# Performance work log

Measured on AMD Instinct MI355X. Metric: run time of the kernel, lower is better.

## Reference

```python
import jax, jax.numpy as jnp
import numpy as np

N = 50000      # nodes
E = 800000     # edges (avg degree 16)
D = 256        # d_model
H = 8          # heads
C = D // H     # per-head channels = 32
DE = 64        # edge feature dim
NEG_SLOPE = 0.2
EPS = 1e-5


def setup_inputs() -> dict:
    key = jax.random.key(0)
    ks = jax.random.split(key, 12)
    s = 0.05
    return {
        "x": jax.random.normal(ks[0], (N, D), jnp.float32),
        "edge_attr": jax.random.normal(ks[1], (E, DE), jnp.float32),
        "edge_index": jax.random.randint(ks[2], (2, E), 0, N, dtype=jnp.int32),
        # GATv2Conv params (torch Linear layout: [out, in])
        "W_l": jax.random.normal(ks[3], (H * C, D), jnp.float32) * s,   # lin_l (source)
        "b_l": jnp.zeros((H * C,), jnp.float32),
        "W_r": jax.random.normal(ks[4], (H * C, D), jnp.float32) * s,   # lin_r (target)
        "b_r": jnp.zeros((H * C,), jnp.float32),
        "W_e": jax.random.normal(ks[5], (H * C, DE), jnp.float32) * s,  # lin_edge (no bias)
        "att": jax.random.normal(ks[6], (H, C), jnp.float32) * s,       # attention vector a
        "W_res": jax.random.normal(ks[7], (H * C, D), jnp.float32) * s, # residual Linear (no bias)
        "bias": jnp.zeros((H * C,), jnp.float32),                        # conv output bias
        "gamma": jnp.ones((D,), jnp.float32),                            # LayerNorm weight
        "beta": jnp.zeros((D,), jnp.float32),                            # LayerNorm bias
    }


def reference(x, edge_attr, W_l, b_l, W_r, b_r, W_e, att, W_res, bias, gamma, beta, edge_index):
    src = edge_index[0]  # j (messages flow source -> target)
    dst = edge_index[1]  # i

    xl = (x @ W_l.T + b_l).reshape(N, H, C)   # source transform
    xr = (x @ W_r.T + b_r).reshape(N, H, C)   # target transform
    ee = (edge_attr @ W_e.T).reshape(E, H, C)  # edge embedding

    # GATv2 attention logits per edge/head
    g = jax.nn.leaky_relu(xl[src] + xr[dst] + ee, NEG_SLOPE)  # [E, H, C]
    alpha = jnp.einsum("ehc,hc->eh", g, att)                   # [E, H]

    # segment softmax over incoming edges of each target node
    amax = jax.ops.segment_max(alpha, dst, num_segments=N)     # [N, H] (-inf for empty)
    ealpha = jnp.exp(alpha - amax[dst])
    denom = jax.ops.segment_sum(ealpha, dst, num_segments=N)   # [N, H]
    alpha = ealpha / jnp.where(denom > 0, denom, 1.0)[dst]

    # weighted message aggregation (scatter-add)
    msg = xl[src] * alpha[:, :, None]                          # [E, H, C]
    out = jax.ops.segment_sum(msg, dst, num_segments=N)        # [N, H, C]

    out = out.reshape(N, H * C) + x @ W_res.T + bias           # concat heads + residual + bias

    # LayerNorm over last dim
    mu = out.mean(-1, keepdims=True)
    var = ((out - mu) ** 2).mean(-1, keepdims=True)
    return (out - mu) * jax.lax.rsqrt(var + EPS) * gamma + beta
```

## Files before the change

kernel.cpp:

```cpp
#include <hip/hip_runtime.h>

#define N_NODES 50000
#define N_EDGES 800000
#define D_MODEL 256
#define H_HEADS 8
#define C_CH 32
#define DE_DIM 64
#define NEG_SLOPE 0.2f
#define LN_EPS 1e-5f
#define TILES (N_EDGES / 64)
#define AGG_K 32

typedef float  f32x4  __attribute__((ext_vector_type(4)));
typedef short  bf16x8 __attribute__((ext_vector_type(8)));

static __device__ __forceinline__ unsigned short f2bf(float f) {
    unsigned int u = __float_as_uint(f);
    u += 0x7fffu + ((u >> 16) & 1u);
    return (unsigned short)(u >> 16);
}
static __device__ __forceinline__ float bf2f(unsigned short s) {
    return __uint_as_float(((unsigned int)s) << 16);
}
static __device__ __forceinline__ bf16x8 load_cvt8(const float* __restrict__ p) {
    float4 a = *(const float4*)p;
    float4 b = *(const float4*)(p + 4);
    bf16x8 r;
    r[0] = (short)f2bf(a.x); r[1] = (short)f2bf(a.y);
    r[2] = (short)f2bf(a.z); r[3] = (short)f2bf(a.w);
    r[4] = (short)f2bf(b.x); r[5] = (short)f2bf(b.y);
    r[6] = (short)f2bf(b.z); r[7] = (short)f2bf(b.w);
    return r;
}

__global__ __launch_bounds__(256) void cvt_bf16_kernel(const float* __restrict__ in,
                                                       unsigned short* __restrict__ out,
                                                       int n8) {
    int g = blockIdx.x * 256 + threadIdx.x;
    if (g < n8) {
        bf16x8 v = load_cvt8(in + (size_t)g * 8);
        *(bf16x8*)(out + (size_t)g * 8) = v;
    }
}

__global__ __launch_bounds__(256) void node_gemm(const unsigned short* __restrict__ xbf,
                                                 const unsigned short* __restrict__ Wbf,
                                                 const float* __restrict__ bl,
                                                 const float* __restrict__ br,
                                                 unsigned short* __restrict__ xl,
                                                 unsigned short* __restrict__ xr,
                                                 float* __restrict__ res) {
    int tid = threadIdx.x;
    int lane = tid & 63, wv = tid >> 6;
    int quad = lane >> 4, l15 = lane & 15;
    int rowTile = blockIdx.x * 64;
    int which = blockIdx.y;
    const unsigned short* W = Wbf + (size_t)which * 65536;
    int colBase = wv * 64;

    f32x4 acc[4][4];
#pragma unroll
    for (int r = 0; r < 4; r++)
#pragma unroll
        for (int c = 0; c < 4; c++) acc[r][c] = (f32x4){0.f, 0.f, 0.f, 0.f};

#pragma unroll 1
    for (int k8 = 0; k8 < 8; ++k8) {
        int kb = k8 * 32 + quad * 8;
        bf16x8 af[4], bfr[4];
#pragma unroll
        for (int r = 0; r < 4; r++) {
            int row = rowTile + r * 16 + l15;
            if (row > N_NODES - 1) row = N_NODES - 1;
            af[r] = *(const bf16x8*)(xbf + (size_t)row * D_MODEL + kb);
        }
#pragma unroll
        for (int c = 0; c < 4; c++) {
            int col = colBase + c * 16 + l15;
            bfr[c] = *(const bf16x8*)(W + (size_t)col * D_MODEL + kb);
        }
#pragma unroll
        for (int r = 0; r < 4; r++)
#pragma unroll
            for (int c = 0; c < 4; c++)
                acc[r][c] = __builtin_amdgcn_mfma_f32_16x16x32_bf16(af[r], bfr[c], acc[r][c], 0, 0, 0);
    }

    float bv[4];
#pragma unroll
    for (int c = 0; c < 4; c++) {
        int col = colBase + c * 16 + l15;
        bv[c] = (which == 0) ? bl[col] : (which == 1 ? br[col] : 0.f);
    }
#pragma unroll
    for (int r = 0; r < 4; r++) {
#pragma unroll
        for (int g = 0; g < 4; g++) {
            int row = rowTile + r * 16 + quad * 4 + g;
            if (row < N_NODES) {
#pragma unroll
                for (int c = 0; c < 4; c++) {
                    int col = colBase + c * 16 + l15;
                    float v = acc[r][c][g] + bv[c];
                    size_t idx = (size_t)row * D_MODEL + col;
                    if (which == 0)      xl[idx] = f2bf(v);
                    else if (which == 1) xr[idx] = f2bf(v);
                    else                 res[idx] = v;
                }
            }
        }
    }
}

__global__ __launch_bounds__(256) void edge_logits(const float* __restrict__ edge_attr,
                                                   const float* __restrict__ We,
                                                   const float* __restrict__ att,
                                                   const int* __restrict__ srcIdx,
                                                   const int* __restrict__ dstIdx,
                                                   const int* __restrict__ posOf,
                                                   const unsigned short* __restrict__ xl,
                                                   const unsigned short* __restrict__ xr,
                                                   float* __restrict__ alphaP) {
    __shared__ short weS[2048 * 8];
    __shared__ float attS[256];
    __shared__ short aS[4][128 * 8];

    int tid = threadIdx.x;
    int lane = tid & 63, wv = tid >> 6;
    int quad = lane >> 4, l15 = lane & 15;

    for (int g = tid; g < 2048; g += 256) {
        int c = g >> 7, kq = (g >> 6) & 1, ln = g & 63;
        int o = c * 16 + (ln & 15);
        int k = kq * 32 + (ln >> 4) * 8;
        bf16x8 v = load_cvt8(We + o * DE_DIM + k);
        *(bf16x8*)&weS[g * 8] = v;
    }
    if (tid < 256) attS[tid] = att[tid];
    __syncthreads();

    for (int tile = blockIdx.x; tile < TILES; tile += gridDim.x) {
        int e0 = tile * 64 + wv * 16;
#pragma unroll
        for (int kq = 0; kq < 2; ++kq) {
            int e = e0 + l15;
            int k = kq * 32 + quad * 8;
            bf16x8 v = load_cvt8(edge_attr + (size_t)e * DE_DIM + k);
            *(bf16x8*)&aS[wv][(kq * 64 + lane) * 8] = v;
        }
        int srcv[4], dstv[4], posv[4];
#pragma unroll
        for (int r = 0; r < 4; r++) {
            int e = e0 + quad * 4 + r;
            srcv[r] = srcIdx[e];
            dstv[r] = dstIdx[e];
            posv[r] = posOf[e];
        }
        __syncthreads();

        bf16x8 a0 = *(bf16x8*)&aS[wv][(0 * 64 + lane) * 8];
        bf16x8 a1 = *(bf16x8*)&aS[wv][(1 * 64 + lane) * 8];

        float pa[4][8];
#pragma unroll
        for (int r = 0; r < 4; r++)
#pragma unroll
            for (int h = 0; h < 8; h++) pa[r][h] = 0.f;

#pragma unroll
        for (int c = 0; c < 16; c++) {
            bf16x8 b0 = *(bf16x8*)&weS[((c * 2 + 0) * 64 + lane) * 8];
            bf16x8 b1 = *(bf16x8*)&weS[((c * 2 + 1) * 64 + lane) * 8];
            f32x4 ee = (f32x4){0.f, 0.f, 0.f, 0.f};
            ee = __builtin_amdgcn_mfma_f32_16x16x32_bf16(a0, b0, ee, 0, 0, 0);
            ee = __builtin_amdgcn_mfma_f32_16x16x32_bf16(a1, b1, ee, 0, 0, 0);
            int col = c * 16 + l15;
            float attv = attS[col];
#pragma unroll
            for (int r = 0; r < 4; r++) {
                float xlv = bf2f(xl[(size_t)srcv[r] * D_MODEL + col]);
                float xrv = bf2f(xr[(size_t)dstv[r] * D_MODEL + col]);
                float t = ee[r] + xlv + xrv;
                t = (t > 0.f) ? t : NEG_SLOPE * t;
                pa[r][c >> 1] += t * attv;
            }
        }
#pragma unroll
        for (int r = 0; r < 4; r++)
#pragma unroll
            for (int h = 0; h < 8; h++) {
                float v = pa[r][h];
                v += __shfl_xor(v, 1);
                v += __shfl_xor(v, 2);
                v += __shfl_xor(v, 4);
                v += __shfl_xor(v, 8);
                pa[r][h] = v;
            }
        if (l15 == 0) {
#pragma unroll
            for (int r = 0; r < 4; r++) {
#pragma unroll
                for (int h = 0; h < 8; h++)
                    alphaP[(size_t)posv[r] * 8 + h] = pa[r][h];
            }
        }
        __syncthreads();
    }
}

__global__ __launch_bounds__(256) void hist_kernel(const int* __restrict__ dstIdx,
                                                   int* __restrict__ cnt) {
    int e = blockIdx.x * 256 + threadIdx.x;
    if (e < N_EDGES) atomicAdd(&cnt[dstIdx[e]], 1);
}

__global__ __launch_bounds__(1024) void scan_kernel(const int* __restrict__ cnt,
                                                    int* __restrict__ off,
                                                    int* __restrict__ woff) {
    const int CHUNK = 49;
    int tid = threadIdx.x;
    int base = tid * CHUNK;
    int local[CHUNK];
    int sum = 0;
#pragma unroll
    for (int j = 0; j < CHUNK; ++j) {
        int idx = base + j;
        int v = (idx < N_NODES) ? cnt[idx] : 0;
        local[j] = sum;
        sum += v;
    }
    int lane = tid & 63, wv = tid >> 6;
    int s = sum;
#pragma unroll
    for (int ofs = 1; ofs < 64; ofs <<= 1) {
        int t2 = __shfl_up(s, ofs);
        if (lane >= ofs) s += t2;
    }
    __shared__ int wsum[16];
    __shared__ int woffS[16];
    if (lane == 63) wsum[wv] = s;
    __syncthreads();
    if (tid == 0) {
        int a = 0;
#pragma unroll
        for (int i = 0; i < 16; ++i) { woffS[i] = a; a += wsum[i]; }
    }
    __syncthreads();
    int excl = woffS[wv] + (s - sum);
#pragma unroll
    for (int j = 0; j < CHUNK; ++j) {
        int idx = base + j;
        if (idx < N_NODES) {
            int v = excl + local[j];
            off[idx] = v;
            woff[idx] = v;
        }
    }
    if (tid == 0) off[N_NODES] = N_EDGES;
}

__global__ __launch_bounds__(256) void scatter_kernel(const int* __restrict__ srcIdx,
                                                      const int* __restrict__ dstIdx,
                                                      int* __restrict__ woff,
                                                      int* __restrict__ posOf,
                                                      int* __restrict__ srcP) {
    int e = blockIdx.x * 256 + threadIdx.x;
    if (e < N_EDGES) {
        int pos = atomicAdd(&woff[dstIdx[e]], 1);
        posOf[e] = pos;
        srcP[pos] = srcIdx[e];
    }
}

__global__ __launch_bounds__(256) void aggregate_ln(const int* __restrict__ off,
                                                    const int* __restrict__ srcP,
                                                    const float* __restrict__ alphaP,
                                                    const unsigned short* __restrict__ xl,
                                                    const float* __restrict__ res,
                                                    const float* __restrict__ biasc,
                                                    const float* __restrict__ gamma,
                                                    const float* __restrict__ beta,
                                                    float* __restrict__ out) {
    int i = blockIdx.x;
    int t = threadIdx.x;
    int h = t >> 5;
    int beg = off[i], end = off[i + 1];

    __shared__ float wS[AGG_K * 8];
    __shared__ int srcS[AGG_K];

    float s = 0.f, acc = 0.f;
    for (int ch = beg; ch < end; ch += AGG_K) {
        int n = min(AGG_K, end - ch);
        __syncthreads();
        if (t < n * 8) wS[t] = __expf(alphaP[(size_t)ch * 8 + t]);
        if (t < n)     srcS[t] = srcP[ch + t];
        __syncthreads();
#pragma unroll 4
        for (int p = 0; p < n; ++p) {
            float w = wS[p * 8 + h];
            s += w;
            acc += w * bf2f(xl[(size_t)srcS[p] * D_MODEL + t]);
        }
    }
    float v = (end > beg) ? (acc / s) : 0.f;
    v += res[(size_t)i * D_MODEL + t] + biasc[t];

    __shared__ float rs[4], rq[4];
    float sum = v, sq = v * v;
#pragma unroll
    for (int msk = 32; msk >= 1; msk >>= 1) {
        sum += __shfl_xor(sum, msk);
        sq  += __shfl_xor(sq, msk);
    }
    int lane = t & 63, wv = t >> 6;
    __syncthreads();
    if (lane == 0) { rs[wv] = sum; rq[wv] = sq; }
    __syncthreads();
    float tot  = rs[0] + rs[1] + rs[2] + rs[3];
    float totq = rq[0] + rq[1] + rq[2] + rq[3];
    float mu  = tot * (1.f / 256.f);
    float var = totq * (1.f / 256.f) - mu * mu;
    var = fmaxf(var, 0.f);
    float inv = rsqrtf(var + LN_EPS);
    out[(size_t)i * D_MODEL + t] = (v - mu) * inv * gamma[t] + beta[t];
}

extern "C" void kernel_launch(void* const* d_in, const int* in_sizes, int n_in,
                              void* d_out, int out_size, void* d_ws, size_t ws_size,
                              hipStream_t stream) {
    const float* x         = (const float*)d_in[0];
    const float* edge_attr = (const float*)d_in[1];
    const int*   edge_index= (const int*)d_in[2];
    const float* Wl        = (const float*)d_in[3];
    const float* bl        = (const float*)d_in[4];
    const float* Wr        = (const float*)d_in[5];
    const float* br        = (const float*)d_in[6];
    const float* We        = (const float*)d_in[7];
    const float* att       = (const float*)d_in[8];
    const float* Wres      = (const float*)d_in[9];
    const float* biasc     = (const float*)d_in[10];
    const float* gamma     = (const float*)d_in[11];
    const float* beta      = (const float*)d_in[12];
    const int* srcIdx = edge_index;
    const int* dstIdx = edge_index + N_EDGES;
    float* out = (float*)d_out;

    char* ws = (char*)d_ws;
    unsigned short* xl  = (unsigned short*)ws;
    unsigned short* xr  = xl + (size_t)N_NODES * D_MODEL;
    unsigned short* xbf = xr + (size_t)N_NODES * D_MODEL;
    unsigned short* Wbf = xbf + (size_t)N_NODES * D_MODEL;
    float* res    = (float*)(Wbf + 3 * 65536);
    float* alphaP = res + (size_t)N_NODES * D_MODEL;
    int* cnt   = (int*)(alphaP + (size_t)N_EDGES * 8);
    int* off   = cnt + N_NODES;
    int* woff  = off + (N_NODES + 1);
    int* posOf = woff + N_NODES;
    int* srcP  = posOf + N_EDGES;
    (void)ws_size; (void)n_in; (void)in_sizes; (void)out_size;

    hipMemsetAsync(cnt, 0, N_NODES * sizeof(int), stream);

    cvt_bf16_kernel<<<(N_NODES * D_MODEL / 8 + 255) / 256, 256, 0, stream>>>(x, xbf, N_NODES * D_MODEL / 8);
    cvt_bf16_kernel<<<32, 256, 0, stream>>>(Wl,   Wbf,             65536 / 8);
    cvt_bf16_kernel<<<32, 256, 0, stream>>>(Wr,   Wbf + 65536,     65536 / 8);
    cvt_bf16_kernel<<<32, 256, 0, stream>>>(Wres, Wbf + 2 * 65536, 65536 / 8);

    dim3 g1((N_NODES + 63) / 64, 3);
    node_gemm<<<g1, 256, 0, stream>>>(xbf, Wbf, bl, br, xl, xr, res);

    hist_kernel<<<(N_EDGES + 255) / 256, 256, 0, stream>>>(dstIdx, cnt);
    scan_kernel<<<1, 1024, 0, stream>>>(cnt, off, woff);
    scatter_kernel<<<(N_EDGES + 255) / 256, 256, 0, stream>>>(srcIdx, dstIdx, woff, posOf, srcP);

    edge_logits<<<1280, 256, 0, stream>>>(edge_attr, We, att, srcIdx, dstIdx, posOf, xl, xr, alphaP);

    aggregate_ln<<<N_NODES, 256, 0, stream>>>(off, srcP, alphaP, xl, res,
                                              biasc, gamma, beta, out);
}
```

Baseline: 887.4 us.

## Swap MFMA operands in edge_logits to drop LDS staging and syncs

```diff
diff --git a/kernel.cpp b/kernel.cpp
--- a/kernel.cpp
+++ b/kernel.cpp
@@ -123,7 +123,6 @@
                                                    float* __restrict__ alphaP) {
     __shared__ short weS[2048 * 8];
     __shared__ float attS[256];
-    __shared__ short aS[4][128 * 8];
 
     int tid = threadIdx.x;
     int lane = tid & 63, wv = tid >> 6;
@@ -141,70 +140,49 @@
 
     for (int tile = blockIdx.x; tile < TILES; tile += gridDim.x) {
         int e0 = tile * 64 + wv * 16;
-#pragma unroll
-        for (int kq = 0; kq < 2; ++kq) {
-            int e = e0 + l15;
-            int k = kq * 32 + quad * 8;
-            bf16x8 v = load_cvt8(edge_attr + (size_t)e * DE_DIM + k);
-            *(bf16x8*)&aS[wv][(kq * 64 + lane) * 8] = v;
-        }
-        int srcv[4], dstv[4], posv[4];
-#pragma unroll
-        for (int r = 0; r < 4; r++) {
-            int e = e0 + quad * 4 + r;
-            srcv[r] = srcIdx[e];
-            dstv[r] = dstIdx[e];
-            posv[r] = posOf[e];
-        }
-        __syncthreads();
-
-        bf16x8 a0 = *(bf16x8*)&aS[wv][(0 * 64 + lane) * 8];
-        bf16x8 a1 = *(bf16x8*)&aS[wv][(1 * 64 + lane) * 8];
-
-        float pa[4][8];
-#pragma unroll
-        for (int r = 0; r < 4; r++)
-#pragma unroll
-            for (int h = 0; h < 8; h++) pa[r][h] = 0.f;
+        int e = e0 + l15;
+        bf16x8 a0 = load_cvt8(edge_attr + (size_t)e * DE_DIM + quad * 8);
+        bf16x8 a1 = load_cvt8(edge_attr + (size_t)e * DE_DIM + 32 + quad * 8);
+        int se = srcIdx[e];
+        int de = dstIdx[e];
+        int pos = posOf[e];
+        const unsigned short* xlr = xl + (size_t)se * D_MODEL;
+        const unsigned short* xrr = xr + (size_t)de * D_MODEL;
+
+        float pa[8];
+#pragma unroll
+        for (int h = 0; h < 8; h++) pa[h] = 0.f;
 
 #pragma unroll
         for (int c = 0; c < 16; c++) {
             bf16x8 b0 = *(bf16x8*)&weS[((c * 2 + 0) * 64 + lane) * 8];
             bf16x8 b1 = *(bf16x8*)&weS[((c * 2 + 1) * 64 + lane) * 8];
             f32x4 ee = (f32x4){0.f, 0.f, 0.f, 0.f};
-            ee = __builtin_amdgcn_mfma_f32_16x16x32_bf16(a0, b0, ee, 0, 0, 0);
-            ee = __builtin_amdgcn_mfma_f32_16x16x32_bf16(a1, b1, ee, 0, 0, 0);
-            int col = c * 16 + l15;
-            float attv = attS[col];
-#pragma unroll
-            for (int r = 0; r < 4; r++) {
-                float xlv = bf2f(xl[(size_t)srcv[r] * D_MODEL + col]);
-                float xrv = bf2f(xr[(size_t)dstv[r] * D_MODEL + col]);
-                float t = ee[r] + xlv + xrv;
-                t = (t > 0.f) ? t : NEG_SLOPE * t;
-                pa[r][c >> 1] += t * attv;
-            }
-        }
-#pragma unroll
-        for (int r = 0; r < 4; r++)
-#pragma unroll
-            for (int h = 0; h < 8; h++) {
-                float v = pa[r][h];
-                v += __shfl_xor(v, 1);
-                v += __shfl_xor(v, 2);
-                v += __shfl_xor(v, 4);
-                v += __shfl_xor(v, 8);
-                pa[r][h] = v;
-            }
-        if (l15 == 0) {
-#pragma unroll
-            for (int r = 0; r < 4; r++) {
-#pragma unroll
-                for (int h = 0; h < 8; h++)
-                    alphaP[(size_t)posv[r] * 8 + h] = pa[r][h];
-            }
-        }
-        __syncthreads();
+            ee = __builtin_amdgcn_mfma_f32_16x16x32_bf16(b0, a0, ee, 0, 0, 0);
+            ee = __builtin_amdgcn_mfma_f32_16x16x32_bf16(b1, a1, ee, 0, 0, 0);
+            int cb = c * 16 + quad * 4;
+            ushort4 xl4 = *(const ushort4*)(xlr + cb);
+            ushort4 xr4 = *(const ushort4*)(xrr + cb);
+            float4 at4 = *(const float4*)&attS[cb];
+            float t0 = ee[0] + bf2f(xl4.x) + bf2f(xr4.x);
+            float t1 = ee[1] + bf2f(xl4.y) + bf2f(xr4.y);
+            float t2 = ee[2] + bf2f(xl4.z) + bf2f(xr4.z);
+            float t3 = ee[3] + bf2f(xl4.w) + bf2f(xr4.w);
+            t0 = (t0 > 0.f) ? t0 : NEG_SLOPE * t0;
+            t1 = (t1 > 0.f) ? t1 : NEG_SLOPE * t1;
+            t2 = (t2 > 0.f) ? t2 : NEG_SLOPE * t2;
+            t3 = (t3 > 0.f) ? t3 : NEG_SLOPE * t3;
+            pa[c >> 1] += t0 * at4.x + t1 * at4.y + t2 * at4.z + t3 * at4.w;
+        }
+#pragma unroll
+        for (int h = 0; h < 8; h++) {
+            float v = pa[h];
+            v += __shfl_xor(v, 16);
+            v += __shfl_xor(v, 32);
+            pa[h] = v;
+        }
+        float2 wout = make_float2(pa[quad * 2], pa[quad * 2 + 1]);
+        *(float2*)(alphaP + (size_t)pos * 8 + quad * 2) = wout;
     }
 }
 
@@ -374,7 +352,7 @@
     scan_kernel<<<1, 1024, 0, stream>>>(cnt, off, woff);
     scatter_kernel<<<(N_EDGES + 255) / 256, 256, 0, stream>>>(srcIdx, dstIdx, woff, posOf, srcP);
 
-    edge_logits<<<1280, 256, 0, stream>>>(edge_attr, We, att, srcIdx, dstIdx, posOf, xl, xr, alphaP);
+    edge_logits<<<2048, 256, 0, stream>>>(edge_attr, We, att, srcIdx, dstIdx, posOf, xl, xr, alphaP);
 
     aggregate_ln<<<N_NODES, 256, 0, stream>>>(off, srcP, alphaP, xl, res,
                                               biasc, gamma, beta, out);
```

Measured after the change: 1.065 ms. 1.2x slower.
